# Kernel optimization log

Hardware: AMD Instinct MI355X
Metric: run time of the kernel (lower is better)

## Reference

```python
import jax, jax.numpy as jnp
import numpy as np

N_NODES = 50000
N_EDGES = 800000
D = 64
H = 4
ALPHA = 0.2  # LeakyReLU negative slope


def gat_conv(x, W, a_s, a_d, src, dst):
    # x: [N, D], W: [D, D], a_s/a_d: [D]
    h = x @ W                               # [N, D]
    s_src = h @ a_s                         # [N]
    s_dst = h @ a_d                         # [N]
    e = jax.nn.leaky_relu(s_src[src] + s_dst[dst], ALPHA)   # [E]
    # segment softmax over incoming edges of each dst node
    m = jax.ops.segment_max(e, dst, num_segments=N_NODES)   # [N]
    ex = jnp.exp(e - m[dst])                                # [E]
    z = jax.ops.segment_sum(ex, dst, num_segments=N_NODES)  # [N]
    attn = ex / (z[dst] + 1e-16)                            # [E]
    out = jax.ops.segment_sum(h[src] * attn[:, None], dst, num_segments=N_NODES)
    return out


def gat_layer(x, W, a_s, a_d, src, dst):
    # sequential application of H single-head convs (as in the torch code);
    # dropout is identity in eval mode
    out = x
    for i in range(H):
        out = gat_conv(out, W[i], a_s[i], a_d[i], src, dst)
    return jax.nn.elu(out)


def setup_inputs() -> dict:
    key = jax.random.key(0)
    ks = jax.random.split(key, 8)
    sc = 1.0 / np.sqrt(D)
    features = jax.random.normal(ks[0], (N_NODES, D), dtype=jnp.float32)
    edge_index = jax.random.randint(ks[1], (2, N_EDGES), 0, N_NODES, dtype=jnp.int64)
    W1 = jax.random.normal(ks[2], (H, D, D), dtype=jnp.float32) * sc
    a_src1 = jax.random.normal(ks[3], (H, D), dtype=jnp.float32) * sc
    a_dst1 = jax.random.normal(ks[4], (H, D), dtype=jnp.float32) * sc
    W2 = jax.random.normal(ks[5], (H, D, D), dtype=jnp.float32) * sc
    a_src2 = jax.random.normal(ks[6], (H, D), dtype=jnp.float32) * sc
    a_dst2 = jax.random.normal(ks[7], (H, D), dtype=jnp.float32) * sc
    return {"features": features, "edge_index": edge_index,
            "W1": W1, "a_src1": a_src1, "a_dst1": a_dst1,
            "W2": W2, "a_src2": a_src2, "a_dst2": a_dst2}


def reference(features, edge_index, W1, a_src1, a_dst1, W2, a_src2, a_dst2):
    src, dst = edge_index[0], edge_index[1]
    x = gat_layer(features, W1, a_src1, a_dst1, src, dst)
    # F.dropout between layers is identity in eval mode
    x = gat_layer(x, W2, a_src2, a_dst2, src, dst)
    return x
```

## Files before the change

### kernel.cpp

```cpp
#include <hip/hip_runtime.h>
#include <hip/hip_bf16.h>

#define N_NODES 50000
#define N_EDGES 800000
#define DIM 64
#define NB 391
#define NBLK 128
#define CHUNK 6250
#define CAP 4096
#define NTILES 3125

typedef __attribute__((ext_vector_type(8))) short bf16x8;
typedef __attribute__((ext_vector_type(4))) float f32x4;

__device__ __forceinline__ float bf2f(unsigned short u) {
  return __uint_as_float(((unsigned int)u) << 16);
}
__device__ __forceinline__ unsigned short f2bf(float f) {
  unsigned int x = __float_as_uint(f);
  unsigned int r = (x + 0x7fffu + ((x >> 16) & 1u)) >> 16;
  return (unsigned short)r;
}

__global__ void k_detect(const unsigned short* __restrict__ feat,
                         const unsigned int* __restrict__ eidx,
                         int* __restrict__ flags) {
  int lane = threadIdx.x;
  float v = bf2f(feat[2 * lane]);
  bool big = !(fabsf(v) < 1000.0f);
  unsigned long long bb = __ballot(big);
  unsigned int w = eidx[2 * lane + 1];
  unsigned long long bz = __ballot(w == 0u);
  if (lane == 0) {
    flags[0] = (__popcll(bb) < 8) ? 1 : 0;
    flags[1] = (__popcll(bz) == 64) ? 1 : 0;
  }
}

__device__ __forceinline__ int eidx_at(const int* __restrict__ p, int k, int i64) {
  return p[i64 ? (k << 1) : k];
}

__global__ __launch_bounds__(256) void k_wprep(
    const void* __restrict__ W1, const void* __restrict__ A1s,
    const void* __restrict__ A1d, const void* __restrict__ W2,
    const void* __restrict__ A2s, const void* __restrict__ A2d,
    const int* __restrict__ flags, unsigned short* __restrict__ wfH,
    unsigned short* __restrict__ wfL, unsigned short* __restrict__ baf) {
  __shared__ float Wsh[DIM * DIM];
  __shared__ float was[DIM], wad[DIM];
  const int b = blockIdx.x;
  const int t = threadIdx.x;
  const int bf = flags[0];
  const void* Wv = (b < 4) ? W1 : W2;
  const void* av = (b < 4) ? A1s : A2s;
  const void* dv = (b < 4) ? A1d : A2d;
  const int hm = (b < 4) ? b : b - 4;
  for (int i = t; i < DIM * DIM; i += 256)
    Wsh[i] = bf ? bf2f(((const unsigned short*)Wv)[hm * DIM * DIM + i])
                : ((const float*)Wv)[hm * DIM * DIM + i];
  __syncthreads();
  if (t < 128) {
    int k = t & 63, isd = t >> 6;
    const void* aptr = isd ? dv : av;
    float acc = 0.f;
    for (int c = 0; c < DIM; ++c) {
      float a = bf ? bf2f(((const unsigned short*)aptr)[hm * DIM + c])
                   : ((const float*)aptr)[hm * DIM + c];
      acc = fmaf(Wsh[k * DIM + c], a, acc);
    }
    (isd ? wad : was)[k] = acc;
  }
  __syncthreads();
  for (int idx = t; idx < 512; idx += 256) {
    int lane = idx & 63, ks = (idx >> 6) & 1, cb = idx >> 7;
    int g4 = lane >> 4, r16 = lane & 15;
    int fo = (((b * 4 + cb) * 2 + ks) * 64 + lane) * 8;
#pragma unroll
    for (int j = 0; j < 8; ++j) {
      int k = 32 * ks + 8 * g4 + j;
      float w = Wsh[k * DIM + 16 * cb + r16];
      unsigned short hu = f2bf(w);
      wfH[fo + j] = hu;
      wfL[fo + j] = f2bf(w - bf2f(hu));
    }
  }
  for (int idx = t; idx < 128; idx += 256) {
    int lane = idx & 63, ks = idx >> 6;
    int g4 = lane >> 4, r16 = lane & 15;
    int fo = ((b * 2 + ks) * 64 + lane) * 8;
#pragma unroll
    for (int j = 0; j < 8; ++j) {
      int k = 32 * ks + 8 * g4 + j;
      unsigned short u = 0;
      if (r16 < 4) {
        float w_ = (r16 < 2) ? was[k] : wad[k];
        unsigned short uh = f2bf(w_);
        u = (r16 & 1) ? f2bf(w_ - bf2f(uh)) : uh;
      }
      baf[fo + j] = u;
    }
  }
}

__global__ __launch_bounds__(256) void k_split(const void* __restrict__ feat,
                                               const int* __restrict__ flags,
                                               unsigned short* __restrict__ xh,
                                               unsigned short* __restrict__ xl) {
  int i = (blockIdx.x * 256 + threadIdx.x) * 4;
  if (i >= N_NODES * DIM) return;
  if (flags[0]) {
    ushort4 v = *(const ushort4*)((const unsigned short*)feat + i);
    *(ushort4*)(xh + i) = v;
    *(ushort4*)(xl + i) = make_ushort4(0, 0, 0, 0);
  } else {
    float4 f = *(const float4*)((const float*)feat + i);
    ushort4 h4, l4;
    h4.x = f2bf(f.x); l4.x = f2bf(f.x - bf2f(h4.x));
    h4.y = f2bf(f.y); l4.y = f2bf(f.y - bf2f(h4.y));
    h4.z = f2bf(f.z); l4.z = f2bf(f.z - bf2f(h4.z));
    h4.w = f2bf(f.w); l4.w = f2bf(f.w - bf2f(h4.w));
    *(ushort4*)(xh + i) = h4;
    *(ushort4*)(xl + i) = l4;
  }
}

__global__ void k_scan1(const int* __restrict__ in, int* __restrict__ out,
                        int* __restrict__ bsum, int n) {
  __shared__ int sm[256];
  int t = threadIdx.x, b = blockIdx.x, i = b * 256 + t;
  int v = (i < n) ? in[i] : 0;
  sm[t] = v;
  __syncthreads();
  for (int off = 1; off < 256; off <<= 1) {
    int x = (t >= off) ? sm[t - off] : 0;
    __syncthreads();
    sm[t] += x;
    __syncthreads();
  }
  if (i < n) out[i] = sm[t] - v;
  if (t == 255) bsum[b] = sm[t];
}

__global__ void k_scan2(int* __restrict__ bsum, int nb) {
  __shared__ int sm[256];
  int t = threadIdx.x;
  int v = (t < nb) ? bsum[t] : 0;
  sm[t] = v;
  __syncthreads();
  for (int off = 1; off < 256; off <<= 1) {
    int x = (t >= off) ? sm[t - off] : 0;
    __syncthreads();
    sm[t] += x;
    __syncthreads();
  }
  if (t < nb) bsum[t] = sm[t] - v;
}

__global__ void k_scan3(int* __restrict__ out, const int* __restrict__ bsum, int n) {
  int t = threadIdx.x, b = blockIdx.x, i = b * 256 + t;
  if (i < n) out[i] += bsum[b];
}

__global__ __launch_bounds__(256) void k_hist1(const int* __restrict__ eidx,
                                               const int* __restrict__ flags,
                                               int* __restrict__ hist) {
  __shared__ int h[NB];
  int t = threadIdx.x, b = blockIdx.x;
  for (int i = t; i < NB; i += 256) h[i] = 0;
  __syncthreads();
  int i64 = flags[1];
  int lo = b * CHUNK;
  for (int i = t; i < CHUNK; i += 256) {
    int d = eidx_at(eidx, N_EDGES + lo + i, i64);
    atomicAdd(&h[d >> 7], 1);
  }
  __syncthreads();
  for (int i = t; i < NB; i += 256) hist[i * NBLK + b] = h[i];
}

__global__ __launch_bounds__(256) void k_scatter(const int* __restrict__ eidx,
                                                 const int* __restrict__ flags,
                                                 const int* __restrict__ hscan,
                                                 int2* __restrict__ ebuf) {
  __shared__ int cur[NB];
  int t = threadIdx.x, b = blockIdx.x;
  for (int i = t; i < NB; i += 256) cur[i] = hscan[i * NBLK + b];
  __syncthreads();
  int i64 = flags[1];
  int lo = b * CHUNK;
  for (int i = t; i < CHUNK; i += 256) {
    int d = eidx_at(eidx, N_EDGES + lo + i, i64);
    int s = eidx_at(eidx, lo + i, i64);
    int pos = atomicAdd(&cur[d >> 7], 1);
    ebuf[pos] = make_int2(s, d);
  }
}

__global__ __launch_bounds__(256) void k_place(const int2* __restrict__ ebuf,
                                               const int* __restrict__ hscan,
                                               int* __restrict__ rowp,
                                               int* __restrict__ csr) {
  __shared__ int hcnt[128];
  __shared__ int sm[128];
  __shared__ int cur[128];
  __shared__ int lcsr[CAP];
  int t = threadIdx.x, b = blockIdx.x;
  int lo = hscan[b * NBLK];
  int hi = (b + 1 < NB) ? hscan[(b + 1) * NBLK] : N_EDGES;
  if (t < 128) hcnt[t] = 0;
  __syncthreads();
  for (int i = lo + t; i < hi; i += 256) atomicAdd(&hcnt[ebuf[i].y & 127], 1);
  __syncthreads();
  int v = (t < 128) ? hcnt[t] : 0;
  if (t < 128) sm[t] = v;
  __syncthreads();
  for (int off = 1; off < 128; off <<= 1) {
    int x = (t < 128 && t >= off) ? sm[t - off] : 0;
    __syncthreads();
    if (t < 128) sm[t] += x;
    __syncthreads();
  }
  int d0 = b * 128;
  if (t < 128) {
    int excl = sm[t] - v;
    cur[t] = excl;
    int d = d0 + t;
    if (d < N_NODES) rowp[d] = lo + excl;
  }
  if (b == NB - 1 && t == 0) rowp[N_NODES] = N_EDGES;
  __syncthreads();
  int seg_sz = hi - lo;
  if (seg_sz <= CAP) {
    for (int i = lo + t; i < hi; i += 256) {
      int2 pr = ebuf[i];
      int pos = atomicAdd(&cur[pr.y & 127], 1);
      lcsr[pos] = pr.x;
    }
    __syncthreads();
    for (int i = t; i < seg_sz; i += 256) csr[lo + i] = lcsr[i];
  } else {
    for (int i = lo + t; i < hi; i += 256) {
      int2 pr = ebuf[i];
      int pos = atomicAdd(&cur[pr.y & 127], 1);
      csr[lo + pos] = pr.x;
    }
  }
}

__global__ __launch_bounds__(256) void k_gemm(
    const unsigned short* __restrict__ xh, const unsigned short* __restrict__ xl,
    const unsigned short* __restrict__ wfH, const unsigned short* __restrict__ wfL,
    const unsigned short* __restrict__ baf, int mat,
    unsigned short* __restrict__ hb, float* __restrict__ ss,
    float* __restrict__ sd) {
  const int lane = threadIdx.x & 63;
  const int w = blockIdx.x * 4 + (threadIdx.x >> 6);
  const int wtile = w >> 1;
  if (wtile >= NTILES) return;
  const int cbh = (w & 1) * 2;
  const int r16 = lane & 15;
  const int g4 = lane >> 4;
  const int row0 = wtile * 16;

  const bf16x8* WH = (const bf16x8*)wfH;
  const bf16x8* WL = (const bf16x8*)wfL;
  bf16x8 Bh[2][2], Bl[2][2];
#pragma unroll
  for (int c = 0; c < 2; ++c)
#pragma unroll
    for (int ks = 0; ks < 2; ++ks) {
      int fi = ((mat * 4 + cbh + c) * 2 + ks) * 64 + lane;
      Bh[c][ks] = WH[fi];
      Bl[c][ks] = WL[fi];
    }

  bf16x8 Ah[2], Al[2];
#pragma unroll
  for (int ks = 0; ks < 2; ++ks) {
    Ah[ks] = *(const bf16x8*)(xh + (row0 + r16) * DIM + 32 * ks + 8 * g4);
    Al[ks] = *(const bf16x8*)(xl + (row0 + r16) * DIM + 32 * ks + 8 * g4);
  }

  f32x4 acc[2];
#pragma unroll
  for (int c = 0; c < 2; ++c) {
    acc[c] = (f32x4){0.f, 0.f, 0.f, 0.f};
#pragma unroll
    for (int ks = 0; ks < 2; ++ks) {
      acc[c] = __builtin_amdgcn_mfma_f32_16x16x32_bf16(Ah[ks], Bh[c][ks], acc[c], 0, 0, 0);
      acc[c] = __builtin_amdgcn_mfma_f32_16x16x32_bf16(Al[ks], Bh[c][ks], acc[c], 0, 0, 0);
      acc[c] = __builtin_amdgcn_mfma_f32_16x16x32_bf16(Ah[ks], Bl[c][ks], acc[c], 0, 0, 0);
    }
  }

#pragma unroll
  for (int c = 0; c < 2; ++c)
#pragma unroll
    for (int reg = 0; reg < 4; ++reg)
      hb[(row0 + 4 * g4 + reg) * DIM + (cbh + c) * 16 + r16] = f2bf(acc[c][reg]);

  if (cbh == 0) {
    f32x4 acc2 = (f32x4){0.f, 0.f, 0.f, 0.f};
#pragma unroll
    for (int ks = 0; ks < 2; ++ks) {
      bf16x8 Ba = *(const bf16x8*)(baf + ((mat * 2 + ks) * 64 + lane) * 8);
      acc2 = __builtin_amdgcn_mfma_f32_16x16x32_bf16(Ah[ks], Ba, acc2, 0, 0, 0);
      acc2 = __builtin_amdgcn_mfma_f32_16x16x32_bf16(Al[ks], Ba, acc2, 0, 0, 0);
    }
#pragma unroll
    for (int reg = 0; reg < 4; ++reg) {
      float tmp = acc2[reg] + __shfl_xor(acc2[reg], 1);
      int row = row0 + 4 * g4 + reg;
      if (r16 == 0) ss[row] = tmp;
      else if (r16 == 2) sd[row] = tmp;
    }
  }
}

__device__ __forceinline__ void quad_accum(const unsigned short* __restrict__ hb,
                                           const int2* __restrict__ lps, int cl,
                                           int quarter, int c16, float4& acc) {
  const int quads = (cl + 3) >> 2;
#pragma unroll 4
  for (int tt = 0; tt < quads; ++tt) {
    int j = 4 * tt + quarter;
    int2 pv = lps[j];
    float pj = __int_as_float(pv.x);
    int sj = pv.y;
    ushort4 hv = *(const ushort4*)(hb + sj * DIM + 4 * c16);
    acc.x = fmaf(pj, bf2f(hv.x), acc.x);
    acc.y = fmaf(pj, bf2f(hv.y), acc.y);
    acc.z = fmaf(pj, bf2f(hv.z), acc.z);
    acc.w = fmaf(pj, bf2f(hv.w), acc.w);
  }
}

__global__ __launch_bounds__(256) void k_agg(
    const unsigned short* __restrict__ hb, const float* __restrict__ ss,
    const float* __restrict__ sd, const int* __restrict__ rowp,
    const int* __restrict__ csr, unsigned short* __restrict__ outH,
    unsigned short* __restrict__ outL, void* __restrict__ out_final,
    const int* __restrict__ flags, int do_elu, int is_final) {
  __shared__ __align__(16) int2 lps[4][64];
  const int lane = threadIdx.x & 63;
  const int quarter = lane >> 4;
  const int c16 = lane & 15;
  const int w = threadIdx.x >> 6;
  const int node = blockIdx.x * 4 + w;
  const int base = rowp[node];
  const int deg = rowp[node + 1] - base;
  const float sdn = sd[node];

  float4 acc = {0.f, 0.f, 0.f, 0.f};
  float z;
  if (deg <= 64) {
    int s = 0;
    float p = 0.f;
    if (lane < deg) {
      s = csr[base + lane];
      float t = ss[s] + sdn;
      t = (t >= 0.f) ? t : 0.2f * t;
      p = __expf(t);
    }
    lps[w][lane] = make_int2(__float_as_int(p), s);
    z = p;
    __builtin_amdgcn_wave_barrier();
    quad_accum(hb, &lps[w][0], deg, quarter, c16, acc);
#pragma unroll
    for (int off = 32; off > 0; off >>= 1) z += __shfl_xor(z, off);
  } else {
    z = 0.f;
    for (int c = 0; c < deg; c += 64) {
      int j = c + lane;
      float p = 0.f; int s = 0;
      if (j < deg) {
        s = csr[base + j];
        float sc = ss[s] + sdn;
        sc = (sc >= 0.f) ? sc : 0.2f * sc;
        p = __expf(sc);
      }
      lps[w][lane] = make_int2(__float_as_int(p), s);
      __builtin_amdgcn_wave_barrier();
      z += p;
      const int cl = (deg - c < 64) ? (deg - c) : 64;
      quad_accum(hb, &lps[w][0], cl, quarter, c16, acc);
      __builtin_amdgcn_wave_barrier();
    }
#pragma unroll
    for (int off = 32; off > 0; off >>= 1) z += __shfl_xor(z, off);
  }

  acc.x += __shfl_xor(acc.x, 16);
  acc.y += __shfl_xor(acc.y, 16);
  acc.z += __shfl_xor(acc.z, 16);
  acc.w += __shfl_xor(acc.w, 16);
  acc.x += __shfl_xor(acc.x, 32);
  acc.y += __shfl_xor(acc.y, 32);
  acc.z += __shfl_xor(acc.z, 32);
  acc.w += __shfl_xor(acc.w, 32);

  float inv = 1.f / (z + 1e-16f);
  float ox = acc.x * inv, oy = acc.y * inv;
  float oz = acc.z * inv, ow = acc.w * inv;
  if (do_elu) {
    ox = (ox > 0.f) ? ox : expm1f(ox);
    oy = (oy > 0.f) ? oy : expm1f(oy);
    oz = (oz > 0.f) ? oz : expm1f(oz);
    ow = (ow > 0.f) ? ow : expm1f(ow);
  }
  if (quarter == 0) {
    int idx = node * DIM + 4 * c16;
    if (is_final) {
      if (flags[0]) {
        ushort4 o4 = {f2bf(ox), f2bf(oy), f2bf(oz), f2bf(ow)};
        *(ushort4*)((unsigned short*)out_final + idx) = o4;
      } else {
        float4 o4 = {ox, oy, oz, ow};
        *(float4*)((float*)out_final + idx) = o4;
      }
    } else {
      ushort4 h4, l4;
      h4.x = f2bf(ox); l4.x = f2bf(ox - bf2f(h4.x));
      h4.y = f2bf(oy); l4.y = f2bf(oy - bf2f(h4.y));
      h4.z = f2bf(oz); l4.z = f2bf(oz - bf2f(h4.z));
      h4.w = f2bf(ow); l4.w = f2bf(ow - bf2f(h4.w));
      *(ushort4*)(outH + idx) = h4;
      *(ushort4*)(outL + idx) = l4;
    }
  }
}

extern "C" void kernel_launch(void* const* d_in, const int* in_sizes, int n_in,
                              void* d_out, int out_size, void* d_ws, size_t ws_size,
                              hipStream_t stream) {
  const void* feat = d_in[0];
  const int* eidx = (const int*)d_in[1];

  unsigned short* xh0 = (unsigned short*)d_ws;
  unsigned short* xl0 = xh0 + N_NODES * DIM;
  unsigned short* xh1 = xl0 + N_NODES * DIM;
  unsigned short* xl1 = xh1 + N_NODES * DIM;
  unsigned short* hb  = xl1 + N_NODES * DIM;
  unsigned short* wfH = hb + N_NODES * DIM;
  unsigned short* wfL = wfH + 32768;
  unsigned short* baf = wfL + 32768;
  int2* ebuf = (int2*)(baf + 8192);
  float* ssrc = (float*)(ebuf + N_EDGES);
  float* sdst = ssrc + N_NODES;
  int* csr  = (int*)(sdst + N_NODES);
  int* hist = csr + N_EDGES;
  int* hscan = hist + NB * NBLK;
  int* bsum = hscan + NB * NBLK;
  int* rowp = bsum + 256;
  int* flags = rowp + N_NODES + 1;

  const int NH = NB * NBLK;
  const int SBH = (NH + 255) / 256;

  k_detect<<<1, 64, 0, stream>>>((const unsigned short*)feat,
                                 (const unsigned int*)eidx, flags);
  k_wprep<<<8, 256, 0, stream>>>(d_in[2], d_in[3], d_in[4],
                                 d_in[5], d_in[6], d_in[7],
                                 flags, wfH, wfL, baf);
  k_split<<<(N_NODES * DIM / 4 + 255) / 256, 256, 0, stream>>>(feat, flags, xh1, xl1);
  k_hist1<<<NBLK, 256, 0, stream>>>(eidx, flags, hist);
  k_scan1<<<SBH, 256, 0, stream>>>(hist, hscan, bsum, NH);
  k_scan2<<<1, 256, 0, stream>>>(bsum, SBH);
  k_scan3<<<SBH, 256, 0, stream>>>(hscan, bsum, NH);
  k_scatter<<<NBLK, 256, 0, stream>>>(eidx, flags, hscan, ebuf);
  k_place<<<NB, 256, 0, stream>>>(ebuf, hscan, rowp, csr);

  const int GB = (2 * NTILES + 3) / 4;

  const unsigned short* xh = xh1;
  const unsigned short* xl = xl1;
  for (int i = 0; i < 8; ++i) {
    k_gemm<<<GB, 256, 0, stream>>>(xh, xl, wfH, wfL, baf, i, hb, ssrc, sdst);
    int elu = (i == 3 || i == 7) ? 1 : 0;
    int fin = (i == 7) ? 1 : 0;
    unsigned short* oh = (i & 1) ? xh1 : xh0;
    unsigned short* ol = (i & 1) ? xl1 : xl0;
    k_agg<<<N_NODES / 4, 256, 0, stream>>>(hb, ssrc, sdst, rowp, csr, oh, ol,
                                           d_out, flags, elu, fin);
    xh = oh; xl = ol;
  }
}
```

Baseline: 411.2 us.

## Fuse aggregation with the next layer's GEMM in one kernel

Adds k_fused, which aggregates 32 nodes per block into shared memory, splits the result into bf16 hi/lo in registers, and runs the next conv's MFMA GEMM plus attention-score projection directly from it. This removes the round trip of writing and reading the hi/lo x buffers to global memory and cuts the launch count from 16 to 9. Ping-pong h/score buffers replace the single hb. The cost is a block-wide sync per 32 nodes and lower occupancy from 512-thread blocks, so load imbalance across a block's nodes can leave waves idle.

```diff
diff --git a/kernel.cpp b/kernel.cpp
--- a/kernel.cpp
+++ b/kernel.cpp
@@ -9,6 +9,8 @@
 #define CHUNK 6250
 #define CAP 4096
 #define NTILES 3125
+#define FROWS 32
+#define FPAD 68
 
 typedef __attribute__((ext_vector_type(8))) short bf16x8;
 typedef __attribute__((ext_vector_type(4))) float f32x4;
@@ -336,22 +338,41 @@
   }
 }
 
-__global__ __launch_bounds__(256) void k_agg(
+__device__ __forceinline__ void agg_node_big(
+    const unsigned short* __restrict__ hb, const float* __restrict__ ss,
+    float sdn, int base, int deg, const int* __restrict__ csr, int lane,
+    int quarter, int c16, int2* __restrict__ lpw, float4& acc, float& zo) {
+  float z = 0.f;
+  for (int c = 0; c < deg; c += 64) {
+    int j = c + lane;
+    float p = 0.f; int s = 0;
+    if (j < deg) {
+      s = csr[base + j];
+      float sc = ss[s] + sdn;
+      sc = (sc >= 0.f) ? sc : 0.2f * sc;
+      p = __expf(sc);
+    }
+    lpw[lane] = make_int2(__float_as_int(p), s);
+    __builtin_amdgcn_wave_barrier();
+    z += p;
+    const int cl = (deg - c < 64) ? (deg - c) : 64;
+    quad_accum(hb, lpw, cl, quarter, c16, acc);
+    __builtin_amdgcn_wave_barrier();
+  }
+#pragma unroll
+  for (int off = 32; off > 0; off >>= 1) z += __shfl_xor(z, off);
+  zo = z;
+}
+
+__device__ __forceinline__ void agg_core(
     const unsigned short* __restrict__ hb, const float* __restrict__ ss,
     const float* __restrict__ sd, const int* __restrict__ rowp,
-    const int* __restrict__ csr, unsigned short* __restrict__ outH,
-    unsigned short* __restrict__ outL, void* __restrict__ out_final,
-    const int* __restrict__ flags, int do_elu, int is_final) {
-  __shared__ __align__(16) int2 lps[4][64];
-  const int lane = threadIdx.x & 63;
-  const int quarter = lane >> 4;
-  const int c16 = lane & 15;
-  const int w = threadIdx.x >> 6;
-  const int node = blockIdx.x * 4 + w;
+    const int* __restrict__ csr, int node, int lane, int quarter, int c16,
+    int do_elu, int2* __restrict__ lpw, float& ox, float& oy, float& oz,
+    float& ow) {
   const int base = rowp[node];
   const int deg = rowp[node + 1] - base;
   const float sdn = sd[node];
-
   float4 acc = {0.f, 0.f, 0.f, 0.f};
   float z;
   if (deg <= 64) {
@@ -363,34 +384,16 @@
       t = (t >= 0.f) ? t : 0.2f * t;
       p = __expf(t);
     }
-    lps[w][lane] = make_int2(__float_as_int(p), s);
+    lpw[lane] = make_int2(__float_as_int(p), s);
     z = p;
     __builtin_amdgcn_wave_barrier();
-    quad_accum(hb, &lps[w][0], deg, quarter, c16, acc);
+    quad_accum(hb, lpw, deg, quarter, c16, acc);
+    __builtin_amdgcn_wave_barrier();
 #pragma unroll
     for (int off = 32; off > 0; off >>= 1) z += __shfl_xor(z, off);
   } else {
-    z = 0.f;
-    for (int c = 0; c < deg; c += 64) {
-      int j = c + lane;
-      float p = 0.f; int s = 0;
-      if (j < deg) {
-        s = csr[base + j];
-        float sc = ss[s] + sdn;
-        sc = (sc >= 0.f) ? sc : 0.2f * sc;
-        p = __expf(sc);
-      }
-      lps[w][lane] = make_int2(__float_as_int(p), s);
-      __builtin_amdgcn_wave_barrier();
-      z += p;
-      const int cl = (deg - c < 64) ? (deg - c) : 64;
-      quad_accum(hb, &lps[w][0], cl, quarter, c16, acc);
-      __builtin_amdgcn_wave_barrier();
-    }
-#pragma unroll
-    for (int off = 32; off > 0; off >>= 1) z += __shfl_xor(z, off);
-  }
-
+    agg_node_big(hb, ss, sdn, base, deg, csr, lane, quarter, c16, lpw, acc, z);
+  }
   acc.x += __shfl_xor(acc.x, 16);
   acc.y += __shfl_xor(acc.y, 16);
   acc.z += __shfl_xor(acc.z, 16);
@@ -399,34 +402,127 @@
   acc.y += __shfl_xor(acc.y, 32);
   acc.z += __shfl_xor(acc.z, 32);
   acc.w += __shfl_xor(acc.w, 32);
-
   float inv = 1.f / (z + 1e-16f);
-  float ox = acc.x * inv, oy = acc.y * inv;
-  float oz = acc.z * inv, ow = acc.w * inv;
+  ox = acc.x * inv; oy = acc.y * inv;
+  oz = acc.z * inv; ow = acc.w * inv;
   if (do_elu) {
     ox = (ox > 0.f) ? ox : expm1f(ox);
     oy = (oy > 0.f) ? oy : expm1f(oy);
     oz = (oz > 0.f) ? oz : expm1f(oz);
     ow = (ow > 0.f) ? ow : expm1f(ow);
   }
+}
+
+__global__ __launch_bounds__(512) void k_fused(
+    const unsigned short* __restrict__ hb_in, const float* __restrict__ ss_in,
+    const float* __restrict__ sd_in, const int* __restrict__ rowp,
+    const int* __restrict__ csr, const unsigned short* __restrict__ wfH,
+    const unsigned short* __restrict__ wfL, const unsigned short* __restrict__ baf,
+    int mat, int do_elu, unsigned short* __restrict__ hb_out,
+    float* __restrict__ ss_out, float* __restrict__ sd_out) {
+  __shared__ float outT[FROWS][FPAD];
+  __shared__ __align__(16) int2 lps[8][64];
+  const int tid = threadIdx.x;
+  const int lane = tid & 63;
+  const int w = tid >> 6;
+  const int quarter = lane >> 4;
+  const int c16 = lane & 15;
+  const int blk = blockIdx.x;
+
+  for (int j = 0; j < 4; ++j) {
+    const int row = w * 4 + j;
+    const int node = blk * FROWS + row;
+    float ox = 0.f, oy = 0.f, oz = 0.f, ow = 0.f;
+    if (node < N_NODES)
+      agg_core(hb_in, ss_in, sd_in, rowp, csr, node, lane, quarter, c16,
+               do_elu, &lps[w][0], ox, oy, oz, ow);
+    if (quarter == 0) {
+      float4 o4 = {ox, oy, oz, ow};
+      *(float4*)&outT[row][4 * c16] = o4;
+    }
+  }
+  __syncthreads();
+
+  const int t = w >> 2;
+  const int cb = w & 3;
+  const int r16 = c16;
+  const int g4 = quarter;
+
+  bf16x8 Ah[2], Al[2];
+#pragma unroll
+  for (int ks = 0; ks < 2; ++ks) {
+    const float* src = &outT[t * 16 + r16][32 * ks + 8 * g4];
+    float4 f0 = *(const float4*)src;
+    float4 f1 = *(const float4*)(src + 4);
+    float v[8] = {f0.x, f0.y, f0.z, f0.w, f1.x, f1.y, f1.z, f1.w};
+#pragma unroll
+    for (int jj = 0; jj < 8; ++jj) {
+      unsigned short hu = f2bf(v[jj]);
+      Ah[ks][jj] = (short)hu;
+      Al[ks][jj] = (short)f2bf(v[jj] - bf2f(hu));
+    }
+  }
+
+  const bf16x8* WH = (const bf16x8*)wfH;
+  const bf16x8* WL = (const bf16x8*)wfL;
+  f32x4 acc = (f32x4){0.f, 0.f, 0.f, 0.f};
+#pragma unroll
+  for (int ks = 0; ks < 2; ++ks) {
+    int fi = ((mat * 4 + cb) * 2 + ks) * 64 + lane;
+    bf16x8 Bh = WH[fi];
+    bf16x8 Bl = WL[fi];
+    acc = __builtin_amdgcn_mfma_f32_16x16x32_bf16(Ah[ks], Bh, acc, 0, 0, 0);
+    acc = __builtin_amdgcn_mfma_f32_16x16x32_bf16(Al[ks], Bh, acc, 0, 0, 0);
+    acc = __builtin_amdgcn_mfma_f32_16x16x32_bf16(Ah[ks], Bl, acc, 0, 0, 0);
+  }
+#pragma unroll
+  for (int reg = 0; reg < 4; ++reg) {
+    int row = blk * FROWS + t * 16 + 4 * g4 + reg;
+    if (row < N_NODES) hb_out[row * DIM + cb * 16 + r16] = f2bf(acc[reg]);
+  }
+
+  if (cb == 0) {
+    f32x4 acc2 = (f32x4){0.f, 0.f, 0.f, 0.f};
+#pragma unroll
+    for (int ks = 0; ks < 2; ++ks) {
+      bf16x8 Ba = *(const bf16x8*)(baf + ((mat * 2 + ks) * 64 + lane) * 8);
+      acc2 = __builtin_amdgcn_mfma_f32_16x16x32_bf16(Ah[ks], Ba, acc2, 0, 0, 0);
+      acc2 = __builtin_amdgcn_mfma_f32_16x16x32_bf16(Al[ks], Ba, acc2, 0, 0, 0);
+    }
+#pragma unroll
+    for (int reg = 0; reg < 4; ++reg) {
+      float tmp = acc2[reg] + __shfl_xor(acc2[reg], 1);
+      int row = blk * FROWS + t * 16 + 4 * g4 + reg;
+      if (row < N_NODES) {
+        if (r16 == 0) ss_out[row] = tmp;
+        else if (r16 == 2) sd_out[row] = tmp;
+      }
+    }
+  }
+}
+
+__global__ __launch_bounds__(256) void k_agg(
+    const unsigned short* __restrict__ hb, const float* __restrict__ ss,
+    const float* __restrict__ sd, const int* __restrict__ rowp,
+    const int* __restrict__ csr, void* __restrict__ out_final,
+    const int* __restrict__ flags, int do_elu) {
+  __shared__ __align__(16) int2 lps[4][64];
+  const int lane = threadIdx.x & 63;
+  const int quarter = lane >> 4;
+  const int c16 = lane & 15;
+  const int w = threadIdx.x >> 6;
+  const int node = blockIdx.x * 4 + w;
+  float ox, oy, oz, ow;
+  agg_core(hb, ss, sd, rowp, csr, node, lane, quarter, c16, do_elu,
+           &lps[w][0], ox, oy, oz, ow);
   if (quarter == 0) {
     int idx = node * DIM + 4 * c16;
-    if (is_final) {
-      if (flags[0]) {
-        ushort4 o4 = {f2bf(ox), f2bf(oy), f2bf(oz), f2bf(ow)};
-        *(ushort4*)((unsigned short*)out_final + idx) = o4;
-      } else {
-        float4 o4 = {ox, oy, oz, ow};
-        *(float4*)((float*)out_final + idx) = o4;
-      }
+    if (flags[0]) {
+      ushort4 o4 = {f2bf(ox), f2bf(oy), f2bf(oz), f2bf(ow)};
+      *(ushort4*)((unsigned short*)out_final + idx) = o4;
     } else {
-      ushort4 h4, l4;
-      h4.x = f2bf(ox); l4.x = f2bf(ox - bf2f(h4.x));
-      h4.y = f2bf(oy); l4.y = f2bf(oy - bf2f(h4.y));
-      h4.z = f2bf(oz); l4.z = f2bf(oz - bf2f(h4.z));
-      h4.w = f2bf(ow); l4.w = f2bf(ow - bf2f(h4.w));
-      *(ushort4*)(outH + idx) = h4;
-      *(ushort4*)(outL + idx) = l4;
+      float4 o4 = {ox, oy, oz, ow};
+      *(float4*)((float*)out_final + idx) = o4;
     }
   }
 }
@@ -437,18 +533,19 @@
   const void* feat = d_in[0];
   const int* eidx = (const int*)d_in[1];
 
-  unsigned short* xh0 = (unsigned short*)d_ws;
-  unsigned short* xl0 = xh0 + N_NODES * DIM;
-  unsigned short* xh1 = xl0 + N_NODES * DIM;
+  unsigned short* xh1 = (unsigned short*)d_ws;
   unsigned short* xl1 = xh1 + N_NODES * DIM;
-  unsigned short* hb  = xl1 + N_NODES * DIM;
-  unsigned short* wfH = hb + N_NODES * DIM;
+  unsigned short* hbA = xl1 + N_NODES * DIM;
+  unsigned short* hbB = hbA + N_NODES * DIM;
+  unsigned short* wfH = hbB + N_NODES * DIM;
   unsigned short* wfL = wfH + 32768;
   unsigned short* baf = wfL + 32768;
   int2* ebuf = (int2*)(baf + 8192);
-  float* ssrc = (float*)(ebuf + N_EDGES);
-  float* sdst = ssrc + N_NODES;
-  int* csr  = (int*)(sdst + N_NODES);
+  float* ssA = (float*)(ebuf + N_EDGES);
+  float* sdA = ssA + N_NODES;
+  float* ssB = sdA + N_NODES;
+  float* sdB = ssB + N_NODES;
+  int* csr  = (int*)(sdB + N_NODES);
   int* hist = csr + N_EDGES;
   int* hscan = hist + NB * NBLK;
   int* bsum = hscan + NB * NBLK;
@@ -472,17 +569,21 @@
   k_place<<<NB, 256, 0, stream>>>(ebuf, hscan, rowp, csr);
 
   const int GB = (2 * NTILES + 3) / 4;
-
-  const unsigned short* xh = xh1;
-  const unsigned short* xl = xl1;
-  for (int i = 0; i < 8; ++i) {
-    k_gemm<<<GB, 256, 0, stream>>>(xh, xl, wfH, wfL, baf, i, hb, ssrc, sdst);
-    int elu = (i == 3 || i == 7) ? 1 : 0;
-    int fin = (i == 7) ? 1 : 0;
-    unsigned short* oh = (i & 1) ? xh1 : xh0;
-    unsigned short* ol = (i & 1) ? xl1 : xl0;
-    k_agg<<<N_NODES / 4, 256, 0, stream>>>(hb, ssrc, sdst, rowp, csr, oh, ol,
-                                           d_out, flags, elu, fin);
-    xh = oh; xl = ol;
-  }
-}
+  const int FB = (N_NODES + FROWS - 1) / FROWS;
+
+  k_gemm<<<GB, 256, 0, stream>>>(xh1, xl1, wfH, wfL, baf, 0, hbA, ssA, sdA);
+
+  for (int k = 0; k < 7; ++k) {
+    const unsigned short* hin = (k & 1) ? hbB : hbA;
+    const float* sin_ = (k & 1) ? ssB : ssA;
+    const float* din = (k & 1) ? sdB : sdA;
+    unsigned short* hout = (k & 1) ? hbA : hbB;
+    float* sout = (k & 1) ? ssA : ssB;
+    float* dout = (k & 1) ? sdA : sdB;
+    k_fused<<<FB, 512, 0, stream>>>(hin, sin_, din, rowp, csr, wfH, wfL, baf,
+                                    k + 1, (k == 3) ? 1 : 0, hout, sout, dout);
+  }
+
+  k_agg<<<N_NODES / 4, 256, 0, stream>>>(hbB, ssB, sdB, rowp, csr, d_out,
+                                         flags, 1);
+}
```

Result: faster. 363.8 us (-11.5%).
